# Performance work log

Hardware: AMD Instinct MI355X
Metric: run time of the kernel (lower is better)

The kernel has to match this reference:

```python
import jax, jax.numpy as jnp
import numpy as np

H, W = 480, 640
N, Q, K = 128, 8192, 10
MIN_DEPTH = 0.1


def setup_inputs() -> dict:
    key = jax.random.key(0)
    ks = jax.random.split(key, 8)
    pred_depth = jax.random.uniform(ks[0], (1, H, W), jnp.float32, 0.5, 10.0)
    gt_depth = jax.random.uniform(ks[1], (1, H, W), jnp.float32, 0.0, 10.0)
    gt_masks = jax.random.uniform(ks[2], (N, H, W)) > 0.5
    random_mask = jax.random.uniform(ks[3], (N, H, W)) > 0.95  # matches torch.rand>0.95
    k_matrix = jnp.array([[500.0, 0.0, W / 2.0], [0.0, 500.0, H / 2.0], [0.0, 0.0, 1.0]], jnp.float32)
    xq = jax.random.randint(ks[4], (N, Q), 0, H, jnp.int32)
    yq = jax.random.randint(ks[5], (N, Q), 0, W, jnp.int32)
    xp = jax.random.randint(ks[6], (N, K), 0, H, jnp.int32)
    yp = jax.random.randint(ks[7], (N, K), 0, W, jnp.int32)
    return {"pred_depth": pred_depth, "gt_masks": gt_masks, "gt_depth": gt_depth,
            "k_matrix": k_matrix, "random_mask": random_mask,
            "xq": xq, "yq": yq, "xp": xp, "yp": yp}


def reference(pred_depth, gt_masks, gt_depth, k_matrix, random_mask, xq, yq, xp, yp):
    sg = jax.lax.stop_gradient
    d0 = pred_depth[0]  # [H, W]
    fx, fy = k_matrix[0, 0], k_matrix[1, 1]
    u0 = jnp.float32(W // 2)
    v0 = jnp.float32(H // 2)
    u_u0 = jnp.arange(W, dtype=jnp.float32)[None, :] - u0  # [1, W]
    v_v0 = jnp.arange(H, dtype=jnp.float32)[:, None] - v0  # [H, 1]
    # point cloud pw: [H, W, 3]
    px_map = u_u0 * jnp.abs(d0) / fx
    py_map = v_v0 * jnp.abs(d0) / fy
    pw = jnp.stack([px_map, py_map, d0], axis=-1)

    # candidate weights per mask: gt_mask & (rand>0.95) & (gt_depth > min_depth)
    valid = gt_depth[0] > MIN_DEPTH  # [H, W]
    w = (gt_masks & random_mask & valid[None]).astype(jnp.float32)  # [N, H, W]

    # weighted least-squares plane fit z = a*x + b*y + d  (normal equations, same as (A^T A)^-1 A^T b)
    feat = jnp.stack([px_map, py_map, jnp.ones_like(d0)], axis=-1)  # [H, W, 3]
    M = jnp.einsum('nhw,hwi,hwj->nij', w, feat, feat)  # [N, 3, 3]
    rhs = jnp.einsum('nhw,hwi,hw->ni', w, feat, d0)    # [N, 3]
    cnt = w.sum(axis=(1, 2))
    ok = (jnp.abs(jnp.linalg.det(M)) > 1e-8) & (cnt >= 3.0)  # emulate try/except skip
    M_safe = jnp.where(ok[:, None, None], M, jnp.eye(3, dtype=M.dtype))
    fit = sg(jnp.linalg.solve(M_safe, rhs[..., None])[..., 0])  # [N, 3]; detached (numpy in original)
    a, b, d = fit[:, 0:1], fit[:, 1:2], fit[:, 2:3]

    # gather query / propagated point coordinates (detached in original)
    qx = sg(pw[xq, yq, 0])  # [N, Q]
    qy = sg(pw[xq, yq, 1])
    ppx = sg(pw[xp, yp, 0])  # [N, K]
    ppy = sg(pw[xp, yp, 1])
    pd = d0[xp, yp]          # [N, K], grads flow through these depths

    num = a * qx + b * qy + d   # [N, Q]
    den = a * ppx + b * ppy + d  # [N, K]
    vals = num * jnp.mean(pd / den, axis=1, keepdims=True)  # [N, Q]

    # sequential scatter per mask (later masks overwrite earlier, as in the loop)
    def step(out, t):
        xi, yi, vi, oki = t
        cur = out[xi, yi]
        out = out.at[xi, yi].set(jnp.where(oki, vi, cur))
        return out, None

    out, _ = jax.lax.scan(step, d0, (xq, yq, vals, ok))
    return out[None]
```

## Files before the change

kernel.cpp:

```cpp
#include <hip/hip_runtime.h>

#define H_ 480
#define W_ 640
#define HW 307200
#define NN 128
#define QQ 8192
#define KK 10
#define G_ 6
#define PIXB 6144

#define WS_FLAG   0
#define WS_ACC    64
#define WS_ABD    8192
#define WS_VBITS  16384
#define WS_PRIO   65536

__global__ __launch_bounds__(256) void prep_k(const unsigned int* __restrict__ gm,
                                              const float* __restrict__ gtd,
                                              unsigned long long* __restrict__ vbits,
                                              int* __restrict__ prio,
                                              float* __restrict__ acc,
                                              int* __restrict__ flag)
{
    const int pix = blockIdx.x * 256 + threadIdx.x;
    prio[pix] = 0;
    if (pix < NN * 12) acc[pix] = 0.0f;
    const bool v = gtd[pix] > 0.1f;
    const unsigned long long b = __ballot(v);
    if ((threadIdx.x & 63) == 0) vbits[pix >> 6] = b;

    if (blockIdx.x == 0) {
        __shared__ int sf;
        if (threadIdx.x == 0) sf = 0;
        __syncthreads();
        int f = 0;
        for (int i = threadIdx.x; i < 4096; i += 256) {
            const unsigned int w = gm[i];
            if (w == 0x3F800000u) f |= 2;
            else if (w > 1u) f |= 1;
        }
        if (f) atomicOr(&sf, f);
        __syncthreads();
        if (threadIdx.x == 0) *flag = (sf & 2) ? 2 : ((sf & 1) ? 1 : 0);
    }
}

__global__ __launch_bounds__(256) void reduce_k(
    const float* __restrict__ d0,
    const void* __restrict__ gmv,
    const void* __restrict__ rmv,
    const float* __restrict__ km,
    const int* __restrict__ flag,
    const unsigned long long* __restrict__ vbits,
    float* __restrict__ acc)
{
    const int n = blockIdx.y;
    const int base = blockIdx.x * PIXB + (int)threadIdx.x * 4;
    const int fmt = *flag;
    const float rfx = 1.0f / km[0], rfy = 1.0f / km[4];
    const size_t moff = (size_t)n * HW;

    unsigned bitsArr[G_];
    if (fmt == 0) {
        int4 ga[G_], ra[G_];
        #pragma unroll
        for (int g = 0; g < G_; ++g) {
            const int p = base + g * 1024;
            ga[g] = *reinterpret_cast<const int4*>((const int*)gmv + moff + p);
            ra[g] = *reinterpret_cast<const int4*>((const int*)rmv + moff + p);
        }
        #pragma unroll
        for (int g = 0; g < G_; ++g) {
            const unsigned gb = (unsigned)(ga[g].x!=0) | ((unsigned)(ga[g].y!=0)<<1)
                              | ((unsigned)(ga[g].z!=0)<<2) | ((unsigned)(ga[g].w!=0)<<3);
            const unsigned rb = (unsigned)(ra[g].x!=0) | ((unsigned)(ra[g].y!=0)<<1)
                              | ((unsigned)(ra[g].z!=0)<<2) | ((unsigned)(ra[g].w!=0)<<3);
            bitsArr[g] = gb & rb;
        }
    } else if (fmt == 1) {
        unsigned ga[G_], ra[G_];
        #pragma unroll
        for (int g = 0; g < G_; ++g) {
            const int p = base + g * 1024;
            ga[g] = *reinterpret_cast<const unsigned*>((const unsigned char*)gmv + moff + p);
            ra[g] = *reinterpret_cast<const unsigned*>((const unsigned char*)rmv + moff + p);
        }
        #pragma unroll
        for (int g = 0; g < G_; ++g) {
            const unsigned a = ga[g], b = ra[g];
            const unsigned gb = (unsigned)((a&0xFFu)!=0) | ((unsigned)(((a>>8)&0xFFu)!=0)<<1)
                              | ((unsigned)(((a>>16)&0xFFu)!=0)<<2) | ((unsigned)((a>>24)!=0)<<3);
            const unsigned rb = (unsigned)((b&0xFFu)!=0) | ((unsigned)(((b>>8)&0xFFu)!=0)<<1)
                              | ((unsigned)(((b>>16)&0xFFu)!=0)<<2) | ((unsigned)((b>>24)!=0)<<3);
            bitsArr[g] = gb & rb;
        }
    } else {
        float4 ga[G_], ra[G_];
        #pragma unroll
        for (int g = 0; g < G_; ++g) {
            const int p = base + g * 1024;
            ga[g] = *reinterpret_cast<const float4*>((const float*)gmv + moff + p);
            ra[g] = *reinterpret_cast<const float4*>((const float*)rmv + moff + p);
        }
        #pragma unroll
        for (int g = 0; g < G_; ++g) {
            const unsigned gb = (unsigned)(ga[g].x!=0.f) | ((unsigned)(ga[g].y!=0.f)<<1)
                              | ((unsigned)(ga[g].z!=0.f)<<2) | ((unsigned)(ga[g].w!=0.f)<<3);
            const unsigned rb = (unsigned)(ra[g].x!=0.f) | ((unsigned)(ra[g].y!=0.f)<<1)
                              | ((unsigned)(ra[g].z!=0.f)<<2) | ((unsigned)(ra[g].w!=0.f)<<3);
            bitsArr[g] = gb & rb;
        }
    }

    float s0=0.f,s1=0.f,s2=0.f,s3=0.f,s4=0.f,s5=0.f,s6=0.f,s7=0.f,s8=0.f;
    #pragma unroll
    for (int g = 0; g < G_; ++g) {
        const int p0 = base + g * 1024;
        unsigned bits = bitsArr[g] & ((unsigned)(vbits[p0 >> 6] >> (p0 & 63)) & 0xFu);
        if (bits) {
            const float4 dv = *reinterpret_cast<const float4*>(d0 + p0);
            const int r = p0 / W_;
            const int c0 = p0 - r * W_;
            const float pyb = (float)(r - 240) * rfy;
            while (bits) {
                const int j = __ffs(bits) - 1;
                bits &= bits - 1;
                const float d = (j == 0) ? dv.x : (j == 1) ? dv.y : (j == 2) ? dv.z : dv.w;
                const float ad = fabsf(d);
                const float px = (float)(c0 + j - 320) * ad * rfx;
                const float py = pyb * ad;
                s0 += px*px; s1 += px*py; s2 += px;
                s3 += py*py; s4 += py;    s5 += 1.0f;
                s6 += px*d;  s7 += py*d;  s8 += d;
            }
        }
    }

    float s[9] = {s0,s1,s2,s3,s4,s5,s6,s7,s8};
    #pragma unroll
    for (int off = 32; off > 0; off >>= 1) {
        #pragma unroll
        for (int i = 0; i < 9; ++i) s[i] += __shfl_down(s[i], off);
    }
    __shared__ float ls[4][9];
    const int wave = threadIdx.x >> 6, lane = threadIdx.x & 63;
    if (lane == 0) {
        #pragma unroll
        for (int i = 0; i < 9; ++i) ls[wave][i] = s[i];
    }
    __syncthreads();
    if (threadIdx.x == 0) {
        #pragma unroll
        for (int i = 0; i < 9; ++i)
            atomicAdd(&acc[n*12 + i], ls[0][i] + ls[1][i] + ls[2][i] + ls[3][i]);
    }
}

__global__ void solve_k(const float* __restrict__ acc,
                        const float* __restrict__ d0,
                        const float* __restrict__ km,
                        const int* __restrict__ xp,
                        const int* __restrict__ yp,
                        float* __restrict__ abd)
{
    const int n = blockIdx.x * blockDim.x + threadIdx.x;
    if (n >= NN) return;
    const float* s = acc + n * 12;
    const double M00=s[0], M01=s[1], M02=s[2], M11=s[3], M12=s[4], M22=s[5];
    const double r0=s[6], r1=s[7], r2=s[8];
    const double cnt = M22;
    const double c00 = M11*M22 - M12*M12;
    const double c01 = M01*M22 - M12*M02;
    const double c02 = M01*M12 - M11*M02;
    const double det = M00*c00 - M01*c01 + M02*c02;
    const bool ok = (fabs(det) > 1e-8) && (cnt >= 3.0);
    float a = 0.f, b = 0.f, dc = 0.f, scale = 0.f;
    if (ok) {
        const double inv = 1.0 / det;
        const double t1 = r1*M22 - r2*M12;
        const double t2 = M01*r2 - r1*M02;
        const double x0 = (r0*c00 - M01*t1 + M02*(r1*M12 - r2*M11)) * inv;
        const double x1 = (M00*t1 - r0*c01 + M02*t2) * inv;
        const double x2 = (M00*(M11*r2 - r1*M12) - M01*t2 + r0*c02) * inv;
        a = (float)x0; b = (float)x1; dc = (float)x2;
        const float fx = km[0], fy = km[4];
        float sum = 0.0f;
        for (int k = 0; k < KK; ++k) {
            const int xi = xp[n*KK + k], yi = yp[n*KK + k];
            const float dd = d0[xi * W_ + yi];
            const float ad = fabsf(dd);
            const float ppx = (float)(yi - 320) * ad / fx;
            const float ppy = (float)(xi - 240) * ad / fy;
            const float den = a * ppx + b * ppy + dc;
            sum += dd / den;
        }
        scale = sum / (float)KK;
    }
    abd[n*8+0] = a; abd[n*8+1] = b; abd[n*8+2] = dc;
    abd[n*8+3] = scale;
    abd[n*8+4] = ok ? 1.0f : 0.0f;
}

__global__ __launch_bounds__(256) void prio_k(const int* __restrict__ xq,
                                              const int* __restrict__ yq,
                                              const float* __restrict__ abd,
                                              int* __restrict__ prio)
{
    const int idx = (blockIdx.x * 256 + threadIdx.x) * 4;
    const int n = idx >> 13;
    if (abd[n*8+4] == 0.0f) return;
    const int4 xs = *reinterpret_cast<const int4*>(xq + idx);
    const int4 ys = *reinterpret_cast<const int4*>(yq + idx);
    const int np = n + 1;
    atomicMax(prio + xs.x * W_ + ys.x, np);
    atomicMax(prio + xs.y * W_ + ys.y, np);
    atomicMax(prio + xs.z * W_ + ys.z, np);
    atomicMax(prio + xs.w * W_ + ys.w, np);
}

__global__ __launch_bounds__(256) void final_k(const int* __restrict__ prio,
                                               const float* __restrict__ abd,
                                               const float* __restrict__ d0,
                                               const float* __restrict__ km,
                                               float* __restrict__ out)
{
    const int p0 = (blockIdx.x * 256 + threadIdx.x) * 4;
    const int4 pr4 = *reinterpret_cast<const int4*>(prio + p0);
    const float4 dv = *reinterpret_cast<const float4*>(d0 + p0);
    const float rfx = 1.0f / km[0], rfy = 1.0f / km[4];
    const int r = p0 / W_;
    const int c0 = p0 - r * W_;
    const float yv = (float)(r - 240) * rfy;
    const int pr[4] = {pr4.x, pr4.y, pr4.z, pr4.w};
    const float dd[4] = {dv.x, dv.y, dv.z, dv.w};
    float o[4];
    #pragma unroll
    for (int j = 0; j < 4; ++j) {
        float v = dd[j];
        if (pr[j] > 0) {
            const int n = pr[j] - 1;
            const float ad = fabsf(dd[j]);
            const float qx = (float)(c0 + j - 320) * ad * rfx;
            const float qy = yv * ad;
            v = (abd[n*8+0]*qx + abd[n*8+1]*qy + abd[n*8+2]) * abd[n*8+3];
        }
        o[j] = v;
    }
    *reinterpret_cast<float4*>(out + p0) = make_float4(o[0], o[1], o[2], o[3]);
}

extern "C" void kernel_launch(void* const* d_in, const int* in_sizes, int n_in,
                              void* d_out, int out_size, void* d_ws, size_t ws_size,
                              hipStream_t stream)
{
    const float* d0  = (const float*)d_in[0];
    const void*  gm  = d_in[1];
    const float* gtd = (const float*)d_in[2];
    const float* km  = (const float*)d_in[3];
    const void*  rm  = d_in[4];
    const int*   xq  = (const int*)d_in[5];
    const int*   yq  = (const int*)d_in[6];
    const int*   xp  = (const int*)d_in[7];
    const int*   yp  = (const int*)d_in[8];
    float* out = (float*)d_out;
    char*  ws  = (char*)d_ws;

    int* flag = (int*)(ws + WS_FLAG);
    float* acc = (float*)(ws + WS_ACC);
    float* abd = (float*)(ws + WS_ABD);
    unsigned long long* vbits = (unsigned long long*)(ws + WS_VBITS);
    int* prio = (int*)(ws + WS_PRIO);

    prep_k<<<HW / 256, 256, 0, stream>>>((const unsigned int*)gm, gtd, vbits, prio, acc, flag);
    reduce_k<<<dim3(HW / PIXB, NN), 256, 0, stream>>>(d0, gm, rm, km, flag, vbits, acc);
    solve_k<<<2, 64, 0, stream>>>(acc, d0, km, xp, yp, abd);
    prio_k<<<(NN * QQ / 4) / 256, 256, 0, stream>>>(xq, yq, abd, prio);
    final_k<<<(HW / 4) / 256, 256, 0, stream>>>(prio, abd, d0, km, out);
}
```

Baseline: 141.6 us.

## Split mask reduction into bit-packing pass and sparse bit-iterating reduction

Replaces the single fused reduce kernel with two passes. The first packs gt_mask, random_mask and the depth-valid bits into a per-mask bitmap in workspace. The second walks only the set bits to accumulate the 9 normal-equation sums. The aim is to skip the arithmetic on the roughly 97.5% of pixels that are zero and to vectorise the mask reads, at the cost of an extra launch, a bitmap write/read round trip, and divergent per-lane loops. It falls back to the old kernel when the workspace is too small.

Measured after the change: 126.5 us. 1.12x faster.

```diff
diff --git a/kernel.cpp b/kernel.cpp
--- a/kernel.cpp
+++ b/kernel.cpp
@@ -14,6 +14,8 @@
 #define WS_ABD    8192
 #define WS_VBITS  16384
 #define WS_PRIO   65536
+#define WS_PACK   1294336
+#define WS_NEED   (WS_PACK + (size_t)NN * 4800 * 8)
 
 __global__ __launch_bounds__(256) void prep_k(const unsigned int* __restrict__ gm,
                                               const float* __restrict__ gtd,
@@ -42,6 +44,121 @@
         if (f) atomicOr(&sf, f);
         __syncthreads();
         if (threadIdx.x == 0) *flag = (sf & 2) ? 2 : ((sf & 1) ? 1 : 0);
+    }
+}
+
+__global__ __launch_bounds__(256) void compress_k(
+    const void* __restrict__ gmv,
+    const void* __restrict__ rmv,
+    const int* __restrict__ flag,
+    const unsigned long long* __restrict__ vbits,
+    unsigned char* __restrict__ packed)
+{
+    const int n = blockIdx.y;
+    const int fmt = *flag;
+    const unsigned char* __restrict__ vb8 = (const unsigned char*)vbits;
+    unsigned char* __restrict__ outp = packed + (size_t)n * 38400;
+
+    if (fmt == 0) {
+        const int* gp = (const int*)gmv + (size_t)n * HW;
+        const int* rp = (const int*)rmv + (size_t)n * HW;
+        #pragma unroll
+        for (int k = 0; k < 15; ++k) {
+            const int grp = blockIdx.x * 3840 + k * 256 + (int)threadIdx.x;
+            const int px = grp * 8;
+            const int4 a0 = *reinterpret_cast<const int4*>(gp + px);
+            const int4 a1 = *reinterpret_cast<const int4*>(gp + px + 4);
+            const int4 b0 = *reinterpret_cast<const int4*>(rp + px);
+            const int4 b1 = *reinterpret_cast<const int4*>(rp + px + 4);
+            unsigned g8 = (unsigned)(a0.x!=0) | ((unsigned)(a0.y!=0)<<1) | ((unsigned)(a0.z!=0)<<2) | ((unsigned)(a0.w!=0)<<3)
+                        | ((unsigned)(a1.x!=0)<<4) | ((unsigned)(a1.y!=0)<<5) | ((unsigned)(a1.z!=0)<<6) | ((unsigned)(a1.w!=0)<<7);
+            unsigned r8 = (unsigned)(b0.x!=0) | ((unsigned)(b0.y!=0)<<1) | ((unsigned)(b0.z!=0)<<2) | ((unsigned)(b0.w!=0)<<3)
+                        | ((unsigned)(b1.x!=0)<<4) | ((unsigned)(b1.y!=0)<<5) | ((unsigned)(b1.z!=0)<<6) | ((unsigned)(b1.w!=0)<<7);
+            outp[grp] = (unsigned char)(g8 & r8 & vb8[grp]);
+        }
+    } else if (fmt == 1) {
+        const unsigned char* gp = (const unsigned char*)gmv + (size_t)n * HW;
+        const unsigned char* rp = (const unsigned char*)rmv + (size_t)n * HW;
+        #pragma unroll
+        for (int k = 0; k < 15; ++k) {
+            const int grp = blockIdx.x * 3840 + k * 256 + (int)threadIdx.x;
+            const int px = grp * 8;
+            const unsigned long long a = *reinterpret_cast<const unsigned long long*>(gp + px);
+            const unsigned long long b = *reinterpret_cast<const unsigned long long*>(rp + px);
+            unsigned g8 = 0, r8 = 0;
+            #pragma unroll
+            for (int j = 0; j < 8; ++j) {
+                g8 |= (unsigned)(((a >> (8*j)) & 0xFFull) != 0) << j;
+                r8 |= (unsigned)(((b >> (8*j)) & 0xFFull) != 0) << j;
+            }
+            outp[grp] = (unsigned char)(g8 & r8 & vb8[grp]);
+        }
+    } else {
+        const float* gp = (const float*)gmv + (size_t)n * HW;
+        const float* rp = (const float*)rmv + (size_t)n * HW;
+        #pragma unroll
+        for (int k = 0; k < 15; ++k) {
+            const int grp = blockIdx.x * 3840 + k * 256 + (int)threadIdx.x;
+            const int px = grp * 8;
+            const float4 a0 = *reinterpret_cast<const float4*>(gp + px);
+            const float4 a1 = *reinterpret_cast<const float4*>(gp + px + 4);
+            const float4 b0 = *reinterpret_cast<const float4*>(rp + px);
+            const float4 b1 = *reinterpret_cast<const float4*>(rp + px + 4);
+            unsigned g8 = (unsigned)(a0.x!=0.f) | ((unsigned)(a0.y!=0.f)<<1) | ((unsigned)(a0.z!=0.f)<<2) | ((unsigned)(a0.w!=0.f)<<3)
+                        | ((unsigned)(a1.x!=0.f)<<4) | ((unsigned)(a1.y!=0.f)<<5) | ((unsigned)(a1.z!=0.f)<<6) | ((unsigned)(a1.w!=0.f)<<7);
+            unsigned r8 = (unsigned)(b0.x!=0.f) | ((unsigned)(b0.y!=0.f)<<1) | ((unsigned)(b0.z!=0.f)<<2) | ((unsigned)(b0.w!=0.f)<<3)
+                        | ((unsigned)(b1.x!=0.f)<<4) | ((unsigned)(b1.y!=0.f)<<5) | ((unsigned)(b1.z!=0.f)<<6) | ((unsigned)(b1.w!=0.f)<<7);
+            outp[grp] = (unsigned char)(g8 & r8 & vb8[grp]);
+        }
+    }
+}
+
+__global__ __launch_bounds__(192) void reduce2_k(
+    const float* __restrict__ d0,
+    const unsigned long long* __restrict__ packed,
+    const float* __restrict__ km,
+    float* __restrict__ acc)
+{
+    const int n = blockIdx.y;
+    const int w = blockIdx.x * 192 + (int)threadIdx.x;
+    unsigned long long bits = packed[(size_t)n * 4800 + w];
+    const float rfx = 1.0f / km[0], rfy = 1.0f / km[4];
+
+    float s0=0.f,s1=0.f,s2=0.f,s3=0.f,s4=0.f,s5=0.f,s6=0.f,s7=0.f,s8=0.f;
+    if (bits) {
+        const int r = w / 10;
+        const int c0 = (w - r * 10) * 64;
+        const float pyb = (float)(r - 240) * rfy;
+        const float* drow = d0 + r * W_ + c0;
+        while (bits) {
+            const int j = __ffsll((unsigned long long)bits) - 1;
+            bits &= bits - 1;
+            const float d = drow[j];
+            const float ad = fabsf(d);
+            const float px = (float)(c0 + j - 320) * ad * rfx;
+            const float py = pyb * ad;
+            s0 += px*px; s1 += px*py; s2 += px;
+            s3 += py*py; s4 += py;    s5 += 1.0f;
+            s6 += px*d;  s7 += py*d;  s8 += d;
+        }
+    }
+
+    float s[9] = {s0,s1,s2,s3,s4,s5,s6,s7,s8};
+    #pragma unroll
+    for (int off = 32; off > 0; off >>= 1) {
+        #pragma unroll
+        for (int i = 0; i < 9; ++i) s[i] += __shfl_down(s[i], off);
+    }
+    __shared__ float ls[3][9];
+    const int wave = threadIdx.x >> 6, lane = threadIdx.x & 63;
+    if (lane == 0) {
+        #pragma unroll
+        for (int i = 0; i < 9; ++i) ls[wave][i] = s[i];
+    }
+    __syncthreads();
+    if (threadIdx.x < 9) {
+        const int i = threadIdx.x;
+        atomicAdd(&acc[n*12 + i], ls[0][i] + ls[1][i] + ls[2][i]);
     }
 }
 
@@ -270,9 +387,15 @@
     float* abd = (float*)(ws + WS_ABD);
     unsigned long long* vbits = (unsigned long long*)(ws + WS_VBITS);
     int* prio = (int*)(ws + WS_PRIO);
+    unsigned char* packed = (unsigned char*)(ws + WS_PACK);
 
     prep_k<<<HW / 256, 256, 0, stream>>>((const unsigned int*)gm, gtd, vbits, prio, acc, flag);
-    reduce_k<<<dim3(HW / PIXB, NN), 256, 0, stream>>>(d0, gm, rm, km, flag, vbits, acc);
+    if (ws_size >= WS_NEED) {
+        compress_k<<<dim3(10, NN), 256, 0, stream>>>(gm, rm, flag, vbits, packed);
+        reduce2_k<<<dim3(25, NN), 192, 0, stream>>>(d0, (const unsigned long long*)packed, km, acc);
+    } else {
+        reduce_k<<<dim3(HW / PIXB, NN), 256, 0, stream>>>(d0, gm, rm, km, flag, vbits, acc);
+    }
     solve_k<<<2, 64, 0, stream>>>(acc, d0, km, xp, yp, abd);
     prio_k<<<(NN * QQ / 4) / 256, 256, 0, stream>>>(xq, yq, abd, prio);
     final_k<<<(HW / 4) / 256, 256, 0, stream>>>(prio, abd, d0, km, out);
```

## Restructure mask reduction with per-pixel validity nibbles and nontemporal loads

Applied to the files above, without the earlier changes.

Adds a byte-per-4-pixels validity nibble array written in the prep kernel and rewrites the mask reduction kernel. Each block now loops over 12 coalesced 16-byte chunks per thread with nontemporal loads, and the int and float mask formats share one bitwise-AND path. The final atomic adds are spread over 9 threads instead of one serial thread. The aim is to cut instruction overhead and cache pollution while streaming the large mask tensors. The trade-off is more sequential iterations per thread and less memory-level parallelism than the unrolled batch of 6 loads per thread before.

New measurement: 116.9 us. 1.21x faster.

```diff
diff --git a/kernel.cpp b/kernel.cpp
--- a/kernel.cpp
+++ b/kernel.cpp
@@ -6,18 +6,21 @@
 #define NN 128
 #define QQ 8192
 #define KK 10
-#define G_ 6
-#define PIXB 6144
 
 #define WS_FLAG   0
 #define WS_ACC    64
 #define WS_ABD    8192
 #define WS_VBITS  16384
-#define WS_PRIO   65536
+#define WS_VNIB   57344
+#define WS_PRIO   196608
+#define WS_NEED   (WS_PRIO + (size_t)HW * 4)
+
+typedef unsigned int u32x4 __attribute__((ext_vector_type(4)));
 
 __global__ __launch_bounds__(256) void prep_k(const unsigned int* __restrict__ gm,
                                               const float* __restrict__ gtd,
                                               unsigned long long* __restrict__ vbits,
+                                              unsigned char* __restrict__ vnib,
                                               int* __restrict__ prio,
                                               float* __restrict__ acc,
                                               int* __restrict__ flag)
@@ -27,7 +30,9 @@
     if (pix < NN * 12) acc[pix] = 0.0f;
     const bool v = gtd[pix] > 0.1f;
     const unsigned long long b = __ballot(v);
-    if ((threadIdx.x & 63) == 0) vbits[pix >> 6] = b;
+    const int lane = threadIdx.x & 63;
+    if (lane == 0) vbits[pix >> 6] = b;
+    if ((lane & 3) == 0) vnib[pix >> 2] = (unsigned char)((b >> lane) & 0xFull);
 
     if (blockIdx.x == 0) {
         __shared__ int sf;
@@ -45,79 +50,49 @@
     }
 }
 
-__global__ __launch_bounds__(256) void reduce_k(
+__device__ __forceinline__ unsigned nib4v(const u32x4 a, const u32x4 b)
+{
+    return ((a.x & b.x) ? 1u : 0u) | ((a.y & b.y) ? 2u : 0u)
+         | ((a.z & b.z) ? 4u : 0u) | ((a.w & b.w) ? 8u : 0u);
+}
+
+__global__ __launch_bounds__(256) void reduce3_k(
     const float* __restrict__ d0,
     const void* __restrict__ gmv,
     const void* __restrict__ rmv,
+    const unsigned char* __restrict__ vnib,
+    const int* __restrict__ flag,
     const float* __restrict__ km,
-    const int* __restrict__ flag,
-    const unsigned long long* __restrict__ vbits,
     float* __restrict__ acc)
 {
     const int n = blockIdx.y;
-    const int base = blockIdx.x * PIXB + (int)threadIdx.x * 4;
     const int fmt = *flag;
     const float rfx = 1.0f / km[0], rfy = 1.0f / km[4];
-    const size_t moff = (size_t)n * HW;
-
-    unsigned bitsArr[G_];
-    if (fmt == 0) {
-        int4 ga[G_], ra[G_];
-        #pragma unroll
-        for (int g = 0; g < G_; ++g) {
-            const int p = base + g * 1024;
-            ga[g] = *reinterpret_cast<const int4*>((const int*)gmv + moff + p);
-            ra[g] = *reinterpret_cast<const int4*>((const int*)rmv + moff + p);
-        }
-        #pragma unroll
-        for (int g = 0; g < G_; ++g) {
-            const unsigned gb = (unsigned)(ga[g].x!=0) | ((unsigned)(ga[g].y!=0)<<1)
-                              | ((unsigned)(ga[g].z!=0)<<2) | ((unsigned)(ga[g].w!=0)<<3);
-            const unsigned rb = (unsigned)(ra[g].x!=0) | ((unsigned)(ra[g].y!=0)<<1)
-                              | ((unsigned)(ra[g].z!=0)<<2) | ((unsigned)(ra[g].w!=0)<<3);
-            bitsArr[g] = gb & rb;
-        }
-    } else if (fmt == 1) {
-        unsigned ga[G_], ra[G_];
-        #pragma unroll
-        for (int g = 0; g < G_; ++g) {
-            const int p = base + g * 1024;
-            ga[g] = *reinterpret_cast<const unsigned*>((const unsigned char*)gmv + moff + p);
-            ra[g] = *reinterpret_cast<const unsigned*>((const unsigned char*)rmv + moff + p);
-        }
-        #pragma unroll
-        for (int g = 0; g < G_; ++g) {
-            const unsigned a = ga[g], b = ra[g];
-            const unsigned gb = (unsigned)((a&0xFFu)!=0) | ((unsigned)(((a>>8)&0xFFu)!=0)<<1)
-                              | ((unsigned)(((a>>16)&0xFFu)!=0)<<2) | ((unsigned)((a>>24)!=0)<<3);
-            const unsigned rb = (unsigned)((b&0xFFu)!=0) | ((unsigned)(((b>>8)&0xFFu)!=0)<<1)
-                              | ((unsigned)(((b>>16)&0xFFu)!=0)<<2) | ((unsigned)((b>>24)!=0)<<3);
-            bitsArr[g] = gb & rb;
-        }
-    } else {
-        float4 ga[G_], ra[G_];
-        #pragma unroll
-        for (int g = 0; g < G_; ++g) {
-            const int p = base + g * 1024;
-            ga[g] = *reinterpret_cast<const float4*>((const float*)gmv + moff + p);
-            ra[g] = *reinterpret_cast<const float4*>((const float*)rmv + moff + p);
-        }
-        #pragma unroll
-        for (int g = 0; g < G_; ++g) {
-            const unsigned gb = (unsigned)(ga[g].x!=0.f) | ((unsigned)(ga[g].y!=0.f)<<1)
-                              | ((unsigned)(ga[g].z!=0.f)<<2) | ((unsigned)(ga[g].w!=0.f)<<3);
-            const unsigned rb = (unsigned)(ra[g].x!=0.f) | ((unsigned)(ra[g].y!=0.f)<<1)
-                              | ((unsigned)(ra[g].z!=0.f)<<2) | ((unsigned)(ra[g].w!=0.f)<<3);
-            bitsArr[g] = gb & rb;
-        }
-    }
 
     float s0=0.f,s1=0.f,s2=0.f,s3=0.f,s4=0.f,s5=0.f,s6=0.f,s7=0.f,s8=0.f;
-    #pragma unroll
-    for (int g = 0; g < G_; ++g) {
-        const int p0 = base + g * 1024;
-        unsigned bits = bitsArr[g] & ((unsigned)(vbits[p0 >> 6] >> (p0 & 63)) & 0xFu);
+
+    for (int it = 0; it < 12; ++it) {
+        const int g = blockIdx.x * 3072 + it * 256 + (int)threadIdx.x;
+        unsigned bits;
+        if (fmt != 1) {
+            const u32x4* gp = (const u32x4*)gmv + (size_t)n * (HW/4);
+            const u32x4* rp = (const u32x4*)rmv + (size_t)n * (HW/4);
+            const u32x4 a = __builtin_nontemporal_load(gp + g);
+            const u32x4 b = __builtin_nontemporal_load(rp + g);
+            bits = nib4v(a, b);
+        } else {
+            const unsigned* gp = (const unsigned*)gmv + (size_t)n * (HW/4);
+            const unsigned* rp = (const unsigned*)rmv + (size_t)n * (HW/4);
+            const unsigned ab = __builtin_nontemporal_load(gp + g)
+                              & __builtin_nontemporal_load(rp + g);
+            bits = (unsigned)((ab & 0xFFu) != 0)
+                 | ((unsigned)(((ab >> 8) & 0xFFu) != 0) << 1)
+                 | ((unsigned)(((ab >> 16) & 0xFFu) != 0) << 2)
+                 | ((unsigned)((ab >> 24) != 0) << 3);
+        }
+        bits &= vnib[g];
         if (bits) {
+            const int p0 = g * 4;
             const float4 dv = *reinterpret_cast<const float4*>(d0 + p0);
             const int r = p0 / W_;
             const int c0 = p0 - r * W_;
@@ -149,10 +124,9 @@
         for (int i = 0; i < 9; ++i) ls[wave][i] = s[i];
     }
     __syncthreads();
-    if (threadIdx.x == 0) {
-        #pragma unroll
-        for (int i = 0; i < 9; ++i)
-            atomicAdd(&acc[n*12 + i], ls[0][i] + ls[1][i] + ls[2][i] + ls[3][i]);
+    if (threadIdx.x < 9) {
+        const int i = threadIdx.x;
+        atomicAdd(&acc[n*12 + i], ls[0][i] + ls[1][i] + ls[2][i] + ls[3][i]);
     }
 }
 
@@ -269,10 +243,11 @@
     float* acc = (float*)(ws + WS_ACC);
     float* abd = (float*)(ws + WS_ABD);
     unsigned long long* vbits = (unsigned long long*)(ws + WS_VBITS);
+    unsigned char* vnib = (unsigned char*)(ws + WS_VNIB);
     int* prio = (int*)(ws + WS_PRIO);
 
-    prep_k<<<HW / 256, 256, 0, stream>>>((const unsigned int*)gm, gtd, vbits, prio, acc, flag);
-    reduce_k<<<dim3(HW / PIXB, NN), 256, 0, stream>>>(d0, gm, rm, km, flag, vbits, acc);
+    prep_k<<<HW / 256, 256, 0, stream>>>((const unsigned int*)gm, gtd, vbits, vnib, prio, acc, flag);
+    reduce3_k<<<dim3(25, NN), 256, 0, stream>>>(d0, gm, rm, vnib, flag, km, acc);
     solve_k<<<2, 64, 0, stream>>>(acc, d0, km, xp, yp, abd);
     prio_k<<<(NN * QQ / 4) / 256, 256, 0, stream>>>(xq, yq, abd, prio);
     final_k<<<(HW / 4) / 256, 256, 0, stream>>>(prio, abd, d0, km, out);
```
